# Kernel optimization log

Hardware: AMD Instinct MI355X
Metric: run time of the kernel (lower is better)

Reference implementation:

```python
import jax, jax.numpy as jnp
import numpy as np
from jax import lax

CHUNK = 4
HEADS = 8
SCALE = 16 ** -0.5  # key_dim ** -0.5


def _conv(x, w, pad=0, groups=1):
    return lax.conv_general_dilated(
        x, w, (1, 1), [(pad, pad), (pad, pad)],
        feature_group_count=groups,
        dimension_numbers=('NCHW', 'OIHW', 'NCHW'))


def _bn(x, g, b):
    # eval-mode BatchNorm with unit running stats folded to per-channel affine
    return x * g[:, None, None] + b[:, None, None]


def _shunt_row(x, c):  # torch shunted(..., dim=-1): [B,C,H,W] -> [B,c,C,H]
    B, C, H, W = x.shape
    return x.reshape(B, C, H, W // c, c).transpose(0, 4, 1, 2, 3).mean(-1)


def _shunt_col(x, c):  # torch shunted(..., dim=-2): [B,C,H,W] -> [B,c,C,W]
    B, C, H, W = x.shape
    return x.reshape(B, C, c, H // c, W).transpose(0, 2, 1, 3, 4).mean(-2)


def _posadd(x, pos):
    # F.interpolate(pos, size=N, mode='linear', align_corners=False)
    p = jax.image.resize(pos, (pos.shape[0], pos.shape[1], x.shape[-1]), 'linear')
    return x + p[None]


def _axial(sq, sk, sv, pq, pk):
    # sq/sk: [B,c,nh_kd,L], sv: [B,c,dh,L] -> out [B,c,h,L,d]
    B, c, _, L = sq.shape
    q = _posadd(sq, pq).reshape(B, c, HEADS, -1, L).transpose(0, 1, 2, 4, 3)  # [B,c,h,L,kd]
    k = _posadd(sk, pk).reshape(B, c, HEADS, -1, L)                            # [B,c,h,kd,L]
    v = sv.reshape(B, c, HEADS, -1, L).transpose(0, 1, 2, 4, 3)                # [B,c,h,L,d]
    attn = jax.nn.softmax(jnp.matmul(q, k) * SCALE, axis=-1)
    return jnp.matmul(attn, v)


def _forward(x, wcc, gcc, bcc, wen, gen, ben, sc, wq, gq, bq, wk, gk, bk,
             wv, gv, bv, wd, gd, bd, wp, gp, bp, wr, gr, br,
             wc2, gc2, bc2, wo, go, bo, prq, prk, pcq, pck):
    c = CHUNK
    # conv_ccam_b + ccam_enc
    cb = jax.nn.relu(_bn(_conv(x, wcc, pad=1), gcc, bcc))          # [B,128,H,W]
    cf = jax.nn.relu(_bn(_conv(cb, wen), gen, ben))                # [B,8,H,W]
    B, C, H, W = cb.shape
    # CCAMDec: bmm -> max-subtract -> softmax -> bmm -> scaled residual
    xf = cb.reshape(B, C, H * W)
    yf = cf.reshape(B, cf.shape[1], H * W)
    e = jnp.einsum('bcn,bkn->bck', xf, yf)
    a = jax.nn.softmax(e.max(-1, keepdims=True) - e, axis=-1)
    dec = jnp.einsum('bck,bkn->bcn', a, yf).reshape(B, C, H, W)
    xs = cb + sc[0] * dec
    # qkv projections
    q = _bn(_conv(xs, wq), gq, bq)   # [B,128,H,W]
    k = _bn(_conv(xs, wk), gk, bk)   # [B,128,H,W]
    v = _bn(_conv(xs, wv), gv, bv)   # [B,256,H,W]
    qkv = jnp.concatenate([q, k, v], axis=1)                       # [B,512,H,W]
    qkv = jax.nn.relu(_bn(_conv(qkv, wd, pad=1, groups=512), gd, bd))
    qkv = _bn(_conv(qkv, wp), gp, bp)                              # [B,128,H,W]
    DH = v.shape[1]
    # row axial attention
    xr = _axial(_shunt_row(q, c), _shunt_row(k, c), _shunt_row(v, c), prq, prk)  # [B,c,h,H,d]
    xr = xr.transpose(0, 2, 4, 1, 3).reshape(B, DH, c * c, H // c)
    xr = _bn(_conv(jax.nn.relu(xr), wr), gr, br)[..., None]        # [B,256,16,H/4,1]
    # column axial attention
    xc = _axial(_shunt_col(q, c), _shunt_col(k, c), _shunt_col(v, c), pcq, pck)  # [B,c,h,W,d]
    xc = xc.transpose(0, 2, 4, 1, 3).reshape(B, DH, c * c, W // c)
    xc = _bn(_conv(jax.nn.relu(xc), wc2), gc2, bc2)[:, :, :, None, :]  # [B,256,16,1,W/4]
    xx = (xr + xc).reshape(B, DH, H, W) + v
    # proj + h_sigmoid gate
    att = jnp.clip(_bn(_conv(jax.nn.relu(xx), wo), go, bo) + 3.0, 0.0, 6.0) / 6.0
    return att * qkv


def setup_inputs() -> dict:
    key = jax.random.key(0)
    ks = iter(jax.random.split(key, 40))
    nrm = lambda s, sd=0.05: jax.random.normal(next(ks), s, jnp.float32) * sd
    g = lambda n: 1.0 + 0.02 * jax.random.normal(next(ks), (n,), jnp.float32)
    b = lambda n: 0.02 * jax.random.normal(next(ks), (n,), jnp.float32)
    D, DH, NK = 128, 256, 128
    return dict(
        x=jax.random.normal(next(ks), (8, 64, 128, 128), jnp.float32),
        wcc=nrm((D, 64, 3, 3)), gcc=g(D), bcc=b(D),
        wen=nrm((8, D, 1, 1)), gen=g(8), ben=b(8),
        sc=jnp.array([0.5], jnp.float32),
        wq=nrm((NK, D, 1, 1)), gq=g(NK), bq=b(NK),
        wk=nrm((NK, D, 1, 1)), gk=g(NK), bk=b(NK),
        wv=nrm((DH, D, 1, 1)), gv=g(DH), bv=b(DH),
        wd=nrm((512, 1, 3, 3)), gd=g(512), bd=b(512),
        wp=nrm((D, 512, 1, 1)), gp=g(D), bp=b(D),
        wr=nrm((DH, DH, 1, 1)), gr=g(DH), br=b(DH),
        wc2=nrm((DH, DH, 1, 1)), gc2=g(DH), bc2=b(DH),
        wo=nrm((D, DH, 1, 1)), go=g(D), bo=b(D),
        prq=nrm((4, NK, 16), 1.0), prk=nrm((4, NK, 16), 1.0),
        pcq=nrm((4, NK, 16), 1.0), pck=nrm((4, NK, 16), 1.0),
    )


def reference(x, wcc, gcc, bcc, wen, gen, ben, sc, wq, gq, bq, wk, gk, bk,
              wv, gv, bv, wd, gd, bd, wp, gp, bp, wr, gr, br,
              wc2, gc2, bc2, wo, go, bo, prq, prk, pcq, pck):
    return _forward(x, wcc, gcc, bcc, wen, gen, ben, sc, wq, gq, bq, wk, gk, bk,
                    wv, gv, bv, wd, gd, bd, wp, gp, bp, wr, gr, br,
                    wc2, gc2, bc2, wo, go, bo, prq, prk, pcq, pck)
```

## Files before the change

kernel.cpp:

```cpp
#include <hip/hip_runtime.h>
#include <hip/hip_bf16.h>

typedef unsigned short u16;
typedef unsigned int u32;

#define DEVFN static __device__ __forceinline__

DEVFN float bfu(u32 u) { return __uint_as_float(u << 16); }
DEVFN u16 f2bu(float v) {
  u32 x = __float_as_uint(v);
  return (u16)((x + 0x7fffu + ((x >> 16) & 1u)) >> 16);
}

struct GemmP {
  const float* Xf;
  const float* W; const float* gain; const float* bias;
  float* outF; u16* outH; const float* aux;
  int CI; int N;
  const float* x3;
  const u16* dsrc; const float* wd; const float* gd; const float* bd;
  const float* xrc; const float* xcc;
};

template <int XM, int EP>
__launch_bounds__(256)
__global__ void gemm1x1(GemmP p) {
  __shared__ float Xs[16][64];
  __shared__ float Ws[16][64];
  const int b = blockIdx.z;
  const int n0 = blockIdx.x * 64;
  const int co0 = blockIdx.y * 64;
  const int t = threadIdx.x;
  const int tco = (t >> 4) << 2;
  const int tn = (t & 15) << 2;
  const int lk = t >> 4;
  const int ln = (t & 15) << 2;
  const int wc = t >> 2;
  const int wk = (t & 3) << 2;
  const int CI = p.CI, N = p.N;
  float acc[4][4] = {};

  for (int k0 = 0; k0 < CI; k0 += 16) {
    float v0, v1, v2, v3;
    if constexpr (XM == 0 || XM == 2) {
      const float* src = p.Xf + ((size_t)b * CI + (k0 + lk)) * N + n0 + ln;
      float4 r = *(const float4*)src;
      v0 = r.x; v1 = r.y; v2 = r.z; v3 = r.w;
      if constexpr (XM == 2) {
        v0 = fmaxf(v0, 0.f); v1 = fmaxf(v1, 0.f);
        v2 = fmaxf(v2, 0.f); v3 = fmaxf(v3, 0.f);
      }
    } else if constexpr (XM == 3) {
      const int k = k0 + lk;
      const int ci = k / 9;
      const int tap = k - ci * 9;
      const int dy = tap / 3 - 1;
      const int dx = tap - (tap / 3) * 3 - 1;
      const int y = (n0 >> 7) + dy;
      const int xb = (n0 & 127) + ln + dx;
      const float* src = p.x3 + ((size_t)b * 64 + ci) * 16384 + (size_t)y * 128;
      const bool yok = ((unsigned)y < 128u);
      v0 = (yok && (unsigned)(xb + 0) < 128u) ? src[xb + 0] : 0.f;
      v1 = (yok && (unsigned)(xb + 1) < 128u) ? src[xb + 1] : 0.f;
      v2 = (yok && (unsigned)(xb + 2) < 128u) ? src[xb + 2] : 0.f;
      v3 = (yok && (unsigned)(xb + 3) < 128u) ? src[xb + 3] : 0.f;
    } else if constexpr (XM == 4) {
      const int ci = k0 + lk;
      const int y = n0 >> 7;
      const int xb = (n0 & 127) + ln;
      const u16* src = p.dsrc + ((size_t)b * 512 + ci) * 16384;
      const float* wdp = p.wd + ci * 9;
      float s0 = 0.f, s1 = 0.f, s2 = 0.f, s3 = 0.f;
      #pragma unroll
      for (int dy = -1; dy <= 1; ++dy) {
        const int yy = y + dy;
        if ((unsigned)yy < 128u) {
          float tv[6];
          #pragma unroll
          for (int u = 0; u < 6; ++u) {
            const int xx = xb - 1 + u;
            tv[u] = ((unsigned)xx < 128u) ? bfu((u32)src[(size_t)yy * 128 + xx]) : 0.f;
          }
          const float w0 = wdp[(dy + 1) * 3 + 0];
          const float w1 = wdp[(dy + 1) * 3 + 1];
          const float w2 = wdp[(dy + 1) * 3 + 2];
          s0 += w0 * tv[0] + w1 * tv[1] + w2 * tv[2];
          s1 += w0 * tv[1] + w1 * tv[2] + w2 * tv[3];
          s2 += w0 * tv[2] + w1 * tv[3] + w2 * tv[4];
          s3 += w0 * tv[3] + w1 * tv[4] + w2 * tv[5];
        }
      }
      const float g = p.gd[ci], bb = p.bd[ci];
      v0 = fmaxf(g * s0 + bb, 0.f);
      v1 = fmaxf(g * s1 + bb, 0.f);
      v2 = fmaxf(g * s2 + bb, 0.f);
      v3 = fmaxf(g * s3 + bb, 0.f);
    } else {
      const int ch = k0 + lk;
      const int y = n0 >> 7;
      const int x0i = (n0 & 127) + ln;
      const int cc = y >> 3;
      const int abase = (y & 7) << 2;
      const u16* vsrc = p.dsrc + (((size_t)b * 512 + 256 + ch) * 128 + y) * 128;
      const float* xr = p.xrc + ((size_t)b * 256 + ch) * 512 + cc * 32;
      const float* xc = p.xcc + ((size_t)b * 256 + ch) * 512 + cc * 32;
      uint2 r = *(const uint2*)(vsrc + x0i);
      float vv0 = bfu(r.x & 0xffffu), vv1 = bfu(r.x >> 16);
      float vv2 = bfu(r.y & 0xffffu), vv3 = bfu(r.y >> 16);
      v0 = fmaxf(xr[abase + ((x0i + 0) >> 5)] + xc[(x0i + 0) & 31] + vv0, 0.f);
      v1 = fmaxf(xr[abase + ((x0i + 1) >> 5)] + xc[(x0i + 1) & 31] + vv1, 0.f);
      v2 = fmaxf(xr[abase + ((x0i + 2) >> 5)] + xc[(x0i + 2) & 31] + vv2, 0.f);
      v3 = fmaxf(xr[abase + ((x0i + 3) >> 5)] + xc[(x0i + 3) & 31] + vv3, 0.f);
    }
    Xs[lk][ln + 0] = v0; Xs[lk][ln + 1] = v1;
    Xs[lk][ln + 2] = v2; Xs[lk][ln + 3] = v3;
    {
      const float* src = p.W + (size_t)(co0 + wc) * CI + k0 + wk;
      float4 r = *(const float4*)src;
      Ws[wk + 0][wc] = r.x; Ws[wk + 1][wc] = r.y;
      Ws[wk + 2][wc] = r.z; Ws[wk + 3][wc] = r.w;
    }
    __syncthreads();
    #pragma unroll
    for (int kk = 0; kk < 16; ++kk) {
      const float4 a4 = *(const float4*)&Ws[kk][tco];
      const float4 b4 = *(const float4*)&Xs[kk][tn];
      acc[0][0] += a4.x * b4.x; acc[0][1] += a4.x * b4.y;
      acc[0][2] += a4.x * b4.z; acc[0][3] += a4.x * b4.w;
      acc[1][0] += a4.y * b4.x; acc[1][1] += a4.y * b4.y;
      acc[1][2] += a4.y * b4.z; acc[1][3] += a4.y * b4.w;
      acc[2][0] += a4.z * b4.x; acc[2][1] += a4.z * b4.y;
      acc[2][2] += a4.z * b4.z; acc[2][3] += a4.z * b4.w;
      acc[3][0] += a4.w * b4.x; acc[3][1] += a4.w * b4.y;
      acc[3][2] += a4.w * b4.z; acc[3][3] += a4.w * b4.w;
    }
    __syncthreads();
  }

  const int CO = (int)gridDim.y * 64;
  #pragma unroll
  for (int i = 0; i < 4; ++i) {
    const int co = co0 + tco + i;
    const float g = p.gain[co], bb = p.bias[co];
    const size_t oidx = ((size_t)b * CO + co) * N + n0 + tn;
    float o0 = g * acc[i][0] + bb;
    float o1 = g * acc[i][1] + bb;
    float o2 = g * acc[i][2] + bb;
    float o3 = g * acc[i][3] + bb;
    if constexpr (EP == 3) {
      o0 = fmaxf(o0, 0.f); o1 = fmaxf(o1, 0.f);
      o2 = fmaxf(o2, 0.f); o3 = fmaxf(o3, 0.f);
    }
    if constexpr (EP == 2) {
      const float4 ax = *(const float4*)(p.aux + oidx);
      o0 = fminf(fmaxf(o0 + 3.f, 0.f), 6.f) * (1.f / 6.f) * ax.x;
      o1 = fminf(fmaxf(o1 + 3.f, 0.f), 6.f) * (1.f / 6.f) * ax.y;
      o2 = fminf(fmaxf(o2 + 3.f, 0.f), 6.f) * (1.f / 6.f) * ax.z;
      o3 = fminf(fmaxf(o3 + 3.f, 0.f), 6.f) * (1.f / 6.f) * ax.w;
    }
    if constexpr (EP == 1) {
      u32 wlo = (u32)f2bu(o0) | ((u32)f2bu(o1) << 16);
      u32 whi = (u32)f2bu(o2) | ((u32)f2bu(o3) << 16);
      *(uint2*)(p.outH + oidx) = make_uint2(wlo, whi);
    } else {
      *(float4*)(p.outF + oidx) = make_float4(o0, o1, o2, o3);
    }
  }
}

__global__ void pack_qkv(const float* wq, const float* wk, const float* wv,
                         const float* gq, const float* bq,
                         const float* gk, const float* bk,
                         const float* gv, const float* bv,
                         float* W, float* g, float* b) {
  int t = blockIdx.x * 256 + threadIdx.x;
  if (t < 16384) { W[t] = wq[t]; W[16384 + t] = wk[t]; }
  W[32768 + t] = wv[t];
  if (t < 128) { g[t] = gq[t]; b[t] = bq[t]; g[128 + t] = gk[t]; b[128 + t] = bk[t]; }
  if (t < 256) { g[256 + t] = gv[t]; b[256 + t] = bv[t]; }
}

__global__ void cf_kernel(const float* cb, const float* wen, const float* gen,
                          const float* ben, float* cf) {
  __shared__ float w[8][128];
  const int t = threadIdx.x;
  for (int i = t; i < 1024; i += 256) w[i >> 7][i & 127] = wen[i];
  __syncthreads();
  const int b = blockIdx.y;
  const int n = blockIdx.x * 256 + t;
  const float* xb = cb + (size_t)b * 128 * 16384 + n;
  float acc[8] = {};
  for (int ci = 0; ci < 128; ++ci) {
    const float xv = xb[(size_t)ci * 16384];
    #pragma unroll
    for (int k = 0; k < 8; ++k) acc[k] += w[k][ci] * xv;
  }
  #pragma unroll
  for (int k = 0; k < 8; ++k)
    cf[((size_t)b * 8 + k) * 16384 + n] = fmaxf(gen[k] * acc[k] + ben[k], 0.f);
}

__global__ void ccam_attn(const float* cb, const float* cf, float* a) {
  const int b = blockIdx.x >> 7;
  const int c = blockIdx.x & 127;
  const int t = threadIdx.x;
  const float* xr = cb + ((size_t)b * 128 + c) * 16384;
  const float* yb = cf + (size_t)b * 8 * 16384;
  float pr[8] = {};
  for (int n = t; n < 16384; n += 256) {
    const float xv = xr[n];
    #pragma unroll
    for (int k = 0; k < 8; ++k) pr[k] += xv * yb[k * 16384 + n];
  }
  __shared__ float red[8][256];
  #pragma unroll
  for (int k = 0; k < 8; ++k) red[k][t] = pr[k];
  __syncthreads();
  for (int s = 128; s > 0; s >>= 1) {
    if (t < s) {
      #pragma unroll
      for (int k = 0; k < 8; ++k) red[k][t] += red[k][t + s];
    }
    __syncthreads();
  }
  if (t == 0) {
    float e[8], m = -1e30f;
    #pragma unroll
    for (int k = 0; k < 8; ++k) { e[k] = red[k][0]; m = fmaxf(m, e[k]); }
    float mt = -1e30f;
    #pragma unroll
    for (int k = 0; k < 8; ++k) mt = fmaxf(mt, m - e[k]);
    float s = 0.f, pk[8];
    #pragma unroll
    for (int k = 0; k < 8; ++k) { pk[k] = __expf(m - e[k] - mt); s += pk[k]; }
    const float inv = 1.f / s;
    #pragma unroll
    for (int k = 0; k < 8; ++k) a[((size_t)b * 128 + c) * 8 + k] = pk[k] * inv;
  }
}

__global__ void ccam_apply(float* cb, const float* cf, const float* a, const float* sc) {
  const int bc = blockIdx.y;
  const int b = bc >> 7;
  const int n = blockIdx.x * 256 + threadIdx.x;
  __shared__ float ak[8];
  if (threadIdx.x < 8) ak[threadIdx.x] = a[(size_t)bc * 8 + threadIdx.x];
  __syncthreads();
  const float* yb = cf + (size_t)b * 8 * 16384 + n;
  float dec = 0.f;
  #pragma unroll
  for (int k = 0; k < 8; ++k) dec += ak[k] * yb[k * 16384];
  const size_t idx = (size_t)bc * 16384 + n;
  cb[idx] = cb[idx] + sc[0] * dec;
}

__global__ void shunt_row(const u16* qkv, float* sr) {
  const int idx = blockIdx.x * 256 + threadIdx.x;
  const int h = idx & 127;
  const int c = (idx >> 7) & 511;
  const int b = idx >> 16;
  const uint4* src = (const uint4*)(qkv + (((size_t)b * 512 + c) * 128 + h) * 128);
  float s0 = 0.f, s1 = 0.f, s2 = 0.f, s3 = 0.f;
  #pragma unroll
  for (int w8 = 0; w8 < 16; ++w8) {
    const uint4 u = src[w8];
    s0 += bfu(u.x & 0xffffu) + bfu(u.z & 0xffffu);
    s1 += bfu(u.x >> 16)     + bfu(u.z >> 16);
    s2 += bfu(u.y & 0xffffu) + bfu(u.w & 0xffffu);
    s3 += bfu(u.y >> 16)     + bfu(u.w >> 16);
  }
  const size_t base = (((size_t)b * 4) * 512 + c) * 128 + h;
  sr[base + 0 * 512 * 128] = s0 * (1.f / 32.f);
  sr[base + 1 * 512 * 128] = s1 * (1.f / 32.f);
  sr[base + 2 * 512 * 128] = s2 * (1.f / 32.f);
  sr[base + 3 * 512 * 128] = s3 * (1.f / 32.f);
}

__global__ void shunt_col(const u16* qkv, float* scv) {
  const int idx = blockIdx.x * 256 + threadIdx.x;
  const int w = idx & 127;
  const int c = (idx >> 7) & 511;
  const int jc = (idx >> 16) & 3;
  const int b = idx >> 18;
  const u16* src = qkv + (((size_t)b * 512 + c) * 128 + jc * 32) * 128 + w;
  float s = 0.f;
  #pragma unroll
  for (int hr = 0; hr < 32; ++hr) s += bfu((u32)src[hr * 128]);
  scv[idx] = s * (1.f / 32.f);
}

DEVFN float pinterp(const float* pos, int j, int ch, int col) {
  const float s = (col + 0.5f) * 0.125f - 0.5f;
  const float fl = floorf(s);
  const int i0 = (int)fl;
  const float f = s - fl;
  const int ia = i0 < 0 ? 0 : (i0 > 15 ? 15 : i0);
  const int i1 = i0 + 1;
  const int ib = i1 < 0 ? 0 : (i1 > 15 ? 15 : i1);
  const float* pp = pos + ((size_t)j * 128 + ch) * 16;
  return pp[ia] * (1.f - f) + pp[ib] * f;
}

__global__ void axial(const float* sall, const float* posq, const float* posk,
                      float* out) {
  __shared__ float kl[16][128];
  __shared__ float vl[32][128];
  const int blk = blockIdx.x;
  const int h = blk & 7;
  const int jc = (blk >> 3) & 3;
  const int b = blk >> 5;
  const int r = threadIdx.x;
  const float* base = sall + ((size_t)b * 4 + jc) * 512 * 128;
  for (int i = r; i < 16 * 128; i += 128) {
    const int kd = i >> 7, col = i & 127;
    kl[kd][col] = base[(128 + h * 16 + kd) * 128 + col] + pinterp(posk, jc, h * 16 + kd, col);
  }
  for (int i = r; i < 32 * 128; i += 128) {
    const int d = i >> 7, col = i & 127;
    vl[d][col] = base[(256 + h * 32 + d) * 128 + col];
  }
  __syncthreads();
  float q[16];
  #pragma unroll
  for (int kd = 0; kd < 16; ++kd)
    q[kd] = base[(h * 16 + kd) * 128 + r] + pinterp(posq, jc, h * 16 + kd, r);
  float m = -1e30f;
  for (int col = 0; col < 128; ++col) {
    float s = 0.f;
    #pragma unroll
    for (int kd = 0; kd < 16; ++kd) s += q[kd] * kl[kd][col];
    m = fmaxf(m, s * 0.25f);
  }
  float den = 0.f;
  float acc[32] = {};
  for (int col = 0; col < 128; ++col) {
    float s = 0.f;
    #pragma unroll
    for (int kd = 0; kd < 16; ++kd) s += q[kd] * kl[kd][col];
    const float pv = __expf(s * 0.25f - m);
    den += pv;
    #pragma unroll
    for (int d = 0; d < 32; ++d) acc[d] += pv * vl[d][col];
  }
  const float inv = 1.f / den;
  float* ob = out + ((size_t)b * 256 + h * 32) * 512 + (size_t)jc * 128 + r;
  #pragma unroll
  for (int d = 0; d < 32; ++d) ob[(size_t)d * 512] = acc[d] * inv;
}

extern "C" void kernel_launch(void* const* d_in, const int* in_sizes, int n_in,
                              void* d_out, int out_size, void* d_ws, size_t ws_size,
                              hipStream_t stream) {
  const float* x   = (const float*)d_in[0];
  const float* wcc = (const float*)d_in[1];
  const float* gcc = (const float*)d_in[2];
  const float* bcc = (const float*)d_in[3];
  const float* wen = (const float*)d_in[4];
  const float* gen = (const float*)d_in[5];
  const float* ben = (const float*)d_in[6];
  const float* sc  = (const float*)d_in[7];
  const float* wq  = (const float*)d_in[8];
  const float* gq  = (const float*)d_in[9];
  const float* bq  = (const float*)d_in[10];
  const float* wk  = (const float*)d_in[11];
  const float* gk  = (const float*)d_in[12];
  const float* bk  = (const float*)d_in[13];
  const float* wv  = (const float*)d_in[14];
  const float* gv  = (const float*)d_in[15];
  const float* bv  = (const float*)d_in[16];
  const float* wd  = (const float*)d_in[17];
  const float* gd  = (const float*)d_in[18];
  const float* bd  = (const float*)d_in[19];
  const float* wp  = (const float*)d_in[20];
  const float* gp  = (const float*)d_in[21];
  const float* bp  = (const float*)d_in[22];
  const float* wr  = (const float*)d_in[23];
  const float* gr  = (const float*)d_in[24];
  const float* brr = (const float*)d_in[25];
  const float* wc2 = (const float*)d_in[26];
  const float* gc2 = (const float*)d_in[27];
  const float* bc2 = (const float*)d_in[28];
  const float* wo  = (const float*)d_in[29];
  const float* go  = (const float*)d_in[30];
  const float* bo  = (const float*)d_in[31];
  const float* prq = (const float*)d_in[32];
  const float* prk = (const float*)d_in[33];
  const float* pcq = (const float*)d_in[34];
  const float* pck = (const float*)d_in[35];

  char* ws = (char*)d_ws;
  u16*   qkv     = (u16*)  (ws + 0);
  char*  region  = ws + 134217728;
  float* cb      = (float*)region;
  float* sr_all  = (float*)(region + 0);
  float* sc_all  = (float*)(region + 8388608);
  float* xr_lin  = (float*)(region + 16777216);
  float* xc_lin  = (float*)(region + 20971520);
  float* xr_conv = (float*)(region + 25165824);
  float* xc_conv = (float*)(region + 29360128);
  float* cf      = (float*)(ws + 201326592);
  float* abuf    = (float*)(ws + 205520896);
  float* Wqkv    = (float*)(ws + 205553664);
  float* gqkv    = (float*)(ws + 205815808);
  float* bqkv    = (float*)(ws + 205817856);
  float* qkvp    = (float*)d_out;
  float* out     = (float*)d_out;

  pack_qkv<<<128, 256, 0, stream>>>(wq, wk, wv, gq, bq, gk, bk, gv, bv, Wqkv, gqkv, bqkv);

  { GemmP p{}; p.x3 = x; p.W = wcc; p.gain = gcc; p.bias = bcc; p.outF = cb;
    p.CI = 576; p.N = 16384;
    gemm1x1<3, 3><<<dim3(256, 2, 8), 256, 0, stream>>>(p); }

  cf_kernel<<<dim3(64, 8), 256, 0, stream>>>(cb, wen, gen, ben, cf);

  ccam_attn<<<1024, 256, 0, stream>>>(cb, cf, abuf);
  ccam_apply<<<dim3(64, 1024), 256, 0, stream>>>(cb, cf, abuf, sc);

  { GemmP p{}; p.Xf = cb; p.W = Wqkv; p.gain = gqkv; p.bias = bqkv; p.outH = qkv;
    p.CI = 128; p.N = 16384;
    gemm1x1<0, 1><<<dim3(256, 8, 8), 256, 0, stream>>>(p); }

  shunt_row<<<2048, 256, 0, stream>>>(qkv, sr_all);
  shunt_col<<<8192, 256, 0, stream>>>(qkv, sc_all);

  { GemmP p{}; p.dsrc = qkv; p.wd = wd; p.gd = gd; p.bd = bd;
    p.W = wp; p.gain = gp; p.bias = bp; p.outF = qkvp;
    p.CI = 512; p.N = 16384;
    gemm1x1<4, 0><<<dim3(256, 2, 8), 256, 0, stream>>>(p); }

  axial<<<256, 128, 0, stream>>>(sr_all, prq, prk, xr_lin);
  axial<<<256, 128, 0, stream>>>(sc_all, pcq, pck, xc_lin);

  { GemmP p{}; p.Xf = xr_lin; p.W = wr; p.gain = gr; p.bias = brr; p.outF = xr_conv;
    p.CI = 256; p.N = 512;
    gemm1x1<2, 0><<<dim3(8, 4, 8), 256, 0, stream>>>(p); }
  { GemmP p{}; p.Xf = xc_lin; p.W = wc2; p.gain = gc2; p.bias = bc2; p.outF = xc_conv;
    p.CI = 256; p.N = 512;
    gemm1x1<2, 0><<<dim3(8, 4, 8), 256, 0, stream>>>(p); }

  { GemmP p{}; p.dsrc = qkv; p.xrc = xr_conv; p.xcc = xc_conv;
    p.W = wo; p.gain = go; p.bias = bo; p.aux = qkvp; p.outF = out;
    p.CI = 256; p.N = 16384;
    gemm1x1<5, 2><<<dim3(256, 2, 8), 256, 0, stream>>>(p); }
}
```

Before: 1.724 ms.

## Rewrite pipeline with bf16 MFMA GEMMs and channel-last layout

Replaces the fp32 scalar-FMA 1x1/3x3 conv GEMMs with a bf16 MFMA (16x16x32) kernel and stores all intermediates in channel-last bf16. Weights are pre-packed to bf16, the input is transposed to NHWC, and the depthwise conv gets its own kernel, run per batch ahead of the projection GEMM. The CCAM reductions, shunt and axial kernels are also restructured. It cuts FP32 ALU work and memory traffic but adds bf16 rounding of intermediates and extra launches.

```diff
diff --git a/kernel.cpp b/kernel.cpp
--- a/kernel.cpp
+++ b/kernel.cpp
@@ -3,6 +3,8 @@
 
 typedef unsigned short u16;
 typedef unsigned int u32;
+typedef __attribute__((ext_vector_type(8))) short bf16x8;
+typedef __attribute__((ext_vector_type(4))) float f32x4;
 
 #define DEVFN static __device__ __forceinline__
 
@@ -11,282 +13,346 @@
   u32 x = __float_as_uint(v);
   return (u16)((x + 0x7fffu + ((x >> 16) & 1u)) >> 16);
 }
-
-struct GemmP {
-  const float* Xf;
-  const float* W; const float* gain; const float* bias;
-  float* outF; u16* outH; const float* aux;
-  int CI; int N;
-  const float* x3;
-  const u16* dsrc; const float* wd; const float* gd; const float* bd;
-  const float* xrc; const float* xcc;
+DEVFN float bfe(bf16x8 v, int j) { return bfu((u32)(u16)v[j]); }
+
+struct GP {
+  const u16* X; const u16* W;
+  const u16* Xv; const u16* Xr; const u16* Xc;
+  const u16* auxh;
+  u16* out; float* outf;
+  const float* gain; const float* bias;
+  int K; int NX; int CO; int b0;
 };
 
-template <int XM, int EP>
+template <int LD, int EP, int BM>
 __launch_bounds__(256)
-__global__ void gemm1x1(GemmP p) {
-  __shared__ float Xs[16][64];
-  __shared__ float Ws[16][64];
-  const int b = blockIdx.z;
-  const int n0 = blockIdx.x * 64;
-  const int co0 = blockIdx.y * 64;
+__global__ void gmm(GP p) {
+  __shared__ u16 Ws[64 * 72];
   const int t = threadIdx.x;
-  const int tco = (t >> 4) << 2;
-  const int tn = (t & 15) << 2;
-  const int lk = t >> 4;
-  const int ln = (t & 15) << 2;
-  const int wc = t >> 2;
-  const int wk = (t & 3) << 2;
-  const int CI = p.CI, N = p.N;
-  float acc[4][4] = {};
-
-  for (int k0 = 0; k0 < CI; k0 += 16) {
-    float v0, v1, v2, v3;
-    if constexpr (XM == 0 || XM == 2) {
-      const float* src = p.Xf + ((size_t)b * CI + (k0 + lk)) * N + n0 + ln;
-      float4 r = *(const float4*)src;
-      v0 = r.x; v1 = r.y; v2 = r.z; v3 = r.w;
-      if constexpr (XM == 2) {
-        v0 = fmaxf(v0, 0.f); v1 = fmaxf(v1, 0.f);
-        v2 = fmaxf(v2, 0.f); v3 = fmaxf(v3, 0.f);
-      }
-    } else if constexpr (XM == 3) {
-      const int k = k0 + lk;
-      const int ci = k / 9;
-      const int tap = k - ci * 9;
-      const int dy = tap / 3 - 1;
-      const int dx = tap - (tap / 3) * 3 - 1;
-      const int y = (n0 >> 7) + dy;
-      const int xb = (n0 & 127) + ln + dx;
-      const float* src = p.x3 + ((size_t)b * 64 + ci) * 16384 + (size_t)y * 128;
-      const bool yok = ((unsigned)y < 128u);
-      v0 = (yok && (unsigned)(xb + 0) < 128u) ? src[xb + 0] : 0.f;
-      v1 = (yok && (unsigned)(xb + 1) < 128u) ? src[xb + 1] : 0.f;
-      v2 = (yok && (unsigned)(xb + 2) < 128u) ? src[xb + 2] : 0.f;
-      v3 = (yok && (unsigned)(xb + 3) < 128u) ? src[xb + 3] : 0.f;
-    } else if constexpr (XM == 4) {
-      const int ci = k0 + lk;
-      const int y = n0 >> 7;
-      const int xb = (n0 & 127) + ln;
-      const u16* src = p.dsrc + ((size_t)b * 512 + ci) * 16384;
-      const float* wdp = p.wd + ci * 9;
-      float s0 = 0.f, s1 = 0.f, s2 = 0.f, s3 = 0.f;
-      #pragma unroll
-      for (int dy = -1; dy <= 1; ++dy) {
-        const int yy = y + dy;
+  const int lane = t & 63, wid = t >> 6;
+  const int wn = (wid >> 1) << 6;
+  const int wco = (wid & 1) << 5;
+  const int l15 = lane & 15, lg = lane >> 4;
+  const int n0 = blockIdx.x << 7;
+  const int co0 = blockIdx.y << 6;
+  const int b = (BM == 1) ? 0 : blockIdx.z;
+  const int bo = (BM == 1) ? p.b0 : blockIdx.z;
+  const int K = p.K;
+
+  f32x4 acc[4][2];
+  #pragma unroll
+  for (int f = 0; f < 4; ++f)
+    #pragma unroll
+    for (int c = 0; c < 2; ++c) acc[f][c] = (f32x4){0.f, 0.f, 0.f, 0.f};
+
+  const int sco = t >> 2, sks = (t & 3) << 4;
+  const u16* wrow = p.W + (size_t)(co0 + sco) * K + sks;
+
+  for (int kb = 0; kb < K; kb += 64) {
+    __syncthreads();
+    *(bf16x8*)&Ws[sco * 72 + sks] = *(const bf16x8*)(wrow + kb);
+    *(bf16x8*)&Ws[sco * 72 + sks + 8] = *(const bf16x8*)(wrow + kb + 8);
+    __syncthreads();
+    #pragma unroll
+    for (int ks = 0; ks < 64; ks += 32) {
+      const int k0 = kb + ks;
+      bf16x8 bfr[2];
+      bfr[0] = *(const bf16x8*)&Ws[(wco + l15) * 72 + ks + lg * 8];
+      bfr[1] = *(const bf16x8*)&Ws[(wco + 16 + l15) * 72 + ks + lg * 8];
+      bf16x8 af[4];
+      if constexpr (LD == 0) {
+        const size_t rb = (size_t)(b * p.NX + n0 + wn + l15);
+        #pragma unroll
+        for (int f = 0; f < 4; ++f)
+          af[f] = *(const bf16x8*)(p.X + (rb + f * 16) * K + k0 + lg * 8);
+      } else if constexpr (LD == 1) {
+        const int tap = k0 >> 6;
+        const int dy = tap / 3 - 1, dxt = tap - (tap / 3) * 3 - 1;
+        const int yy = blockIdx.x + dy;
+        const int ci0 = (k0 & 63) + lg * 8;
         if ((unsigned)yy < 128u) {
-          float tv[6];
           #pragma unroll
-          for (int u = 0; u < 6; ++u) {
-            const int xx = xb - 1 + u;
-            tv[u] = ((unsigned)xx < 128u) ? bfu((u32)src[(size_t)yy * 128 + xx]) : 0.f;
+          for (int f = 0; f < 4; ++f) {
+            const int xv = wn + f * 16 + l15 + dxt;
+            bf16x8 t8 = {};
+            if ((unsigned)xv < 128u)
+              t8 = *(const bf16x8*)(p.X + (((size_t)(b * 128 + yy) * 128 + xv) << 6) + ci0);
+            af[f] = t8;
           }
-          const float w0 = wdp[(dy + 1) * 3 + 0];
-          const float w1 = wdp[(dy + 1) * 3 + 1];
-          const float w2 = wdp[(dy + 1) * 3 + 2];
-          s0 += w0 * tv[0] + w1 * tv[1] + w2 * tv[2];
-          s1 += w0 * tv[1] + w1 * tv[2] + w2 * tv[3];
-          s2 += w0 * tv[2] + w1 * tv[3] + w2 * tv[4];
-          s3 += w0 * tv[3] + w1 * tv[4] + w2 * tv[5];
+        } else {
+          #pragma unroll
+          for (int f = 0; f < 4; ++f) af[f] = (bf16x8){};
+        }
+      } else {
+        const int y = blockIdx.x;
+        const int prb = ((y >> 3) << 5) + ((y & 7) << 2);
+        const int pcb = (y >> 3) << 5;
+        const int ch0 = k0 + lg * 8;
+        #pragma unroll
+        for (int f = 0; f < 4; ++f) {
+          const int x = wn + f * 16 + l15;
+          const int nn = n0 + x;
+          bf16x8 v8 = *(const bf16x8*)(p.Xv + ((size_t)(b * 16384 + nn) << 9) + 256 + ch0);
+          bf16x8 r8 = *(const bf16x8*)(p.Xr + ((size_t)(b * 512 + prb + (x >> 5)) << 8) + ch0);
+          bf16x8 c8 = *(const bf16x8*)(p.Xc + ((size_t)(b * 512 + pcb + (x & 31)) << 8) + ch0);
+          bf16x8 av;
+          #pragma unroll
+          for (int j = 0; j < 8; ++j) {
+            float s = bfe(v8, j) + bfe(r8, j) + bfe(c8, j);
+            av[j] = (short)f2bu(fmaxf(s, 0.f));
+          }
+          af[f] = av;
         }
       }
-      const float g = p.gd[ci], bb = p.bd[ci];
-      v0 = fmaxf(g * s0 + bb, 0.f);
-      v1 = fmaxf(g * s1 + bb, 0.f);
-      v2 = fmaxf(g * s2 + bb, 0.f);
-      v3 = fmaxf(g * s3 + bb, 0.f);
-    } else {
-      const int ch = k0 + lk;
-      const int y = n0 >> 7;
-      const int x0i = (n0 & 127) + ln;
-      const int cc = y >> 3;
-      const int abase = (y & 7) << 2;
-      const u16* vsrc = p.dsrc + (((size_t)b * 512 + 256 + ch) * 128 + y) * 128;
-      const float* xr = p.xrc + ((size_t)b * 256 + ch) * 512 + cc * 32;
-      const float* xc = p.xcc + ((size_t)b * 256 + ch) * 512 + cc * 32;
-      uint2 r = *(const uint2*)(vsrc + x0i);
-      float vv0 = bfu(r.x & 0xffffu), vv1 = bfu(r.x >> 16);
-      float vv2 = bfu(r.y & 0xffffu), vv3 = bfu(r.y >> 16);
-      v0 = fmaxf(xr[abase + ((x0i + 0) >> 5)] + xc[(x0i + 0) & 31] + vv0, 0.f);
-      v1 = fmaxf(xr[abase + ((x0i + 1) >> 5)] + xc[(x0i + 1) & 31] + vv1, 0.f);
-      v2 = fmaxf(xr[abase + ((x0i + 2) >> 5)] + xc[(x0i + 2) & 31] + vv2, 0.f);
-      v3 = fmaxf(xr[abase + ((x0i + 3) >> 5)] + xc[(x0i + 3) & 31] + vv3, 0.f);
-    }
-    Xs[lk][ln + 0] = v0; Xs[lk][ln + 1] = v1;
-    Xs[lk][ln + 2] = v2; Xs[lk][ln + 3] = v3;
-    {
-      const float* src = p.W + (size_t)(co0 + wc) * CI + k0 + wk;
-      float4 r = *(const float4*)src;
-      Ws[wk + 0][wc] = r.x; Ws[wk + 1][wc] = r.y;
-      Ws[wk + 2][wc] = r.z; Ws[wk + 3][wc] = r.w;
-    }
-    __syncthreads();
-    #pragma unroll
-    for (int kk = 0; kk < 16; ++kk) {
-      const float4 a4 = *(const float4*)&Ws[kk][tco];
-      const float4 b4 = *(const float4*)&Xs[kk][tn];
-      acc[0][0] += a4.x * b4.x; acc[0][1] += a4.x * b4.y;
-      acc[0][2] += a4.x * b4.z; acc[0][3] += a4.x * b4.w;
-      acc[1][0] += a4.y * b4.x; acc[1][1] += a4.y * b4.y;
-      acc[1][2] += a4.y * b4.z; acc[1][3] += a4.y * b4.w;
-      acc[2][0] += a4.z * b4.x; acc[2][1] += a4.z * b4.y;
-      acc[2][2] += a4.z * b4.z; acc[2][3] += a4.z * b4.w;
-      acc[3][0] += a4.w * b4.x; acc[3][1] += a4.w * b4.y;
-      acc[3][2] += a4.w * b4.z; acc[3][3] += a4.w * b4.w;
-    }
-    __syncthreads();
-  }
-
-  const int CO = (int)gridDim.y * 64;
-  #pragma unroll
-  for (int i = 0; i < 4; ++i) {
-    const int co = co0 + tco + i;
+      #pragma unroll
+      for (int f = 0; f < 4; ++f)
+        #pragma unroll
+        for (int c = 0; c < 2; ++c)
+          acc[f][c] = __builtin_amdgcn_mfma_f32_16x16x32_bf16(af[f], bfr[c], acc[f][c], 0, 0, 0);
+    }
+  }
+
+  #pragma unroll
+  for (int c = 0; c < 2; ++c) {
+    const int co = co0 + wco + (c << 4) + l15;
     const float g = p.gain[co], bb = p.bias[co];
-    const size_t oidx = ((size_t)b * CO + co) * N + n0 + tn;
-    float o0 = g * acc[i][0] + bb;
-    float o1 = g * acc[i][1] + bb;
-    float o2 = g * acc[i][2] + bb;
-    float o3 = g * acc[i][3] + bb;
-    if constexpr (EP == 3) {
-      o0 = fmaxf(o0, 0.f); o1 = fmaxf(o1, 0.f);
-      o2 = fmaxf(o2, 0.f); o3 = fmaxf(o3, 0.f);
-    }
-    if constexpr (EP == 2) {
-      const float4 ax = *(const float4*)(p.aux + oidx);
-      o0 = fminf(fmaxf(o0 + 3.f, 0.f), 6.f) * (1.f / 6.f) * ax.x;
-      o1 = fminf(fmaxf(o1 + 3.f, 0.f), 6.f) * (1.f / 6.f) * ax.y;
-      o2 = fminf(fmaxf(o2 + 3.f, 0.f), 6.f) * (1.f / 6.f) * ax.z;
-      o3 = fminf(fmaxf(o3 + 3.f, 0.f), 6.f) * (1.f / 6.f) * ax.w;
-    }
-    if constexpr (EP == 1) {
-      u32 wlo = (u32)f2bu(o0) | ((u32)f2bu(o1) << 16);
-      u32 whi = (u32)f2bu(o2) | ((u32)f2bu(o3) << 16);
-      *(uint2*)(p.outH + oidx) = make_uint2(wlo, whi);
-    } else {
-      *(float4*)(p.outF + oidx) = make_float4(o0, o1, o2, o3);
-    }
-  }
-}
-
-__global__ void pack_qkv(const float* wq, const float* wk, const float* wv,
-                         const float* gq, const float* bq,
-                         const float* gk, const float* bk,
-                         const float* gv, const float* bv,
-                         float* W, float* g, float* b) {
-  int t = blockIdx.x * 256 + threadIdx.x;
-  if (t < 16384) { W[t] = wq[t]; W[16384 + t] = wk[t]; }
-  W[32768 + t] = wv[t];
-  if (t < 128) { g[t] = gq[t]; b[t] = bq[t]; g[128 + t] = gk[t]; b[128 + t] = bk[t]; }
-  if (t < 256) { g[256 + t] = gv[t]; b[256 + t] = bv[t]; }
-}
-
-__global__ void cf_kernel(const float* cb, const float* wen, const float* gen,
-                          const float* ben, float* cf) {
-  __shared__ float w[8][128];
+    #pragma unroll
+    for (int f = 0; f < 4; ++f) {
+      const int nnb = n0 + wn + (f << 4) + (lg << 2);
+      #pragma unroll
+      for (int r = 0; r < 4; ++r) {
+        float o = g * acc[f][c][r] + bb;
+        const int nn = nnb + r;
+        if constexpr (EP == 1) o = fmaxf(o, 0.f);
+        if constexpr (EP == 2) {
+          o = fminf(fmaxf(o + 3.f, 0.f), 6.f) * (1.f / 6.f);
+          const float q = bfu((u32)p.auxh[((size_t)(bo * 16384 + nn) << 7) + co]);
+          p.outf[((size_t)(bo * 128 + co) << 14) + nn] = o * q;
+        } else {
+          p.out[(size_t)(bo * p.NX + nn) * p.CO + co] = f2bu(o);
+        }
+      }
+    }
+  }
+}
+
+__global__ void pack_k(const float* wcc, const float* wq, const float* wk, const float* wv,
+                       const float* gq, const float* gk, const float* gv,
+                       const float* bq, const float* bk, const float* bv,
+                       const float* wp, const float* wr, const float* wc2, const float* wo,
+                       u16* Wp3, u16* Wqkv, u16* Wwp, u16* Wwr, u16* Wwc, u16* Wwo,
+                       float* gqkv, float* bqkv, float* ebuf) {
+  int i = blockIdx.x * 256 + threadIdx.x;
+  if (i < 73728) {
+    const int co = i / 576, k = i - co * 576;
+    const int tap = k >> 6, ci = k & 63;
+    Wp3[i] = f2bu(wcc[(co * 64 + ci) * 9 + tap]);
+    return;
+  }
+  i -= 73728;
+  if (i < 65536) {
+    const int co = i >> 7, ci = i & 127;
+    const float v = co < 128 ? wq[co * 128 + ci]
+                  : (co < 256 ? wk[(co - 128) * 128 + ci] : wv[(co - 256) * 128 + ci]);
+    Wqkv[i] = f2bu(v);
+    return;
+  }
+  i -= 65536;
+  if (i < 65536) { Wwp[i] = f2bu(wp[i]); return; }
+  i -= 65536;
+  if (i < 65536) { Wwr[i] = f2bu(wr[i]); return; }
+  i -= 65536;
+  if (i < 65536) { Wwc[i] = f2bu(wc2[i]); return; }
+  i -= 65536;
+  if (i < 32768) { Wwo[i] = f2bu(wo[i]); return; }
+  i -= 32768;
+  if (i < 512) { gqkv[i] = i < 128 ? gq[i] : (i < 256 ? gk[i - 128] : gv[i - 256]); return; }
+  i -= 512;
+  if (i < 512) { bqkv[i] = i < 128 ? bq[i] : (i < 256 ? bk[i - 128] : bv[i - 256]); return; }
+  i -= 512;
+  if (i < 8192) ebuf[i] = 0.f;
+}
+
+__global__ void xt_k(const float* x, u16* xt) {
+  __shared__ u16 tile[64 * 130];
+  const int y = blockIdx.x, b = blockIdx.y;
   const int t = threadIdx.x;
-  for (int i = t; i < 1024; i += 256) w[i >> 7][i & 127] = wen[i];
+  {
+    const int ci = t >> 2, xseg = (t & 3) * 32;
+    const float* src = x + ((size_t)(b * 64 + ci) * 128 + y) * 128 + xseg;
+    #pragma unroll
+    for (int j = 0; j < 16; ++j) {
+      const float2 f2 = *(const float2*)(src + j * 2);
+      *(u32*)&tile[ci * 130 + xseg + 2 * j] = (u32)f2bu(f2.x) | ((u32)f2bu(f2.y) << 16);
+    }
+  }
   __syncthreads();
-  const int b = blockIdx.y;
+  const int xx = t >> 1, ch = (t & 1) * 32;
+  u16* dst = xt + (((size_t)(b * 128 + y) * 128 + xx) << 6) + ch;
+  uint4 q0, q1;
+  #pragma unroll
+  for (int h = 0; h < 2; ++h) {
+    const int cb0 = ch + h * 16;
+    u32 w0 = (u32)tile[(cb0 + 0) * 130 + xx] | ((u32)tile[(cb0 + 1) * 130 + xx] << 16);
+    u32 w1 = (u32)tile[(cb0 + 2) * 130 + xx] | ((u32)tile[(cb0 + 3) * 130 + xx] << 16);
+    u32 w2 = (u32)tile[(cb0 + 4) * 130 + xx] | ((u32)tile[(cb0 + 5) * 130 + xx] << 16);
+    u32 w3 = (u32)tile[(cb0 + 6) * 130 + xx] | ((u32)tile[(cb0 + 7) * 130 + xx] << 16);
+    u32 w4 = (u32)tile[(cb0 + 8) * 130 + xx] | ((u32)tile[(cb0 + 9) * 130 + xx] << 16);
+    u32 w5 = (u32)tile[(cb0 + 10) * 130 + xx] | ((u32)tile[(cb0 + 11) * 130 + xx] << 16);
+    u32 w6 = (u32)tile[(cb0 + 12) * 130 + xx] | ((u32)tile[(cb0 + 13) * 130 + xx] << 16);
+    u32 w7 = (u32)tile[(cb0 + 14) * 130 + xx] | ((u32)tile[(cb0 + 15) * 130 + xx] << 16);
+    if (h == 0) { q0 = make_uint4(w0, w1, w2, w3); q1 = make_uint4(w4, w5, w6, w7); }
+    else {
+      *(uint4*)(dst) = q0; *(uint4*)(dst + 8) = q1;
+      *(uint4*)(dst + 16) = make_uint4(w0, w1, w2, w3);
+      *(uint4*)(dst + 24) = make_uint4(w4, w5, w6, w7);
+    }
+  }
+}
+
+__global__ void cf_k(const u16* cb, const float* wen, const float* gen,
+                     const float* ben, u16* cf) {
+  __shared__ float wsm[1024];
+  const int t = threadIdx.x;
+  for (int i = t; i < 1024; i += 256) wsm[i] = wen[i];
+  __syncthreads();
   const int n = blockIdx.x * 256 + t;
-  const float* xb = cb + (size_t)b * 128 * 16384 + n;
+  const u16* row = cb + ((size_t)n << 7);
   float acc[8] = {};
-  for (int ci = 0; ci < 128; ++ci) {
-    const float xv = xb[(size_t)ci * 16384];
-    #pragma unroll
-    for (int k = 0; k < 8; ++k) acc[k] += w[k][ci] * xv;
-  }
-  #pragma unroll
-  for (int k = 0; k < 8; ++k)
-    cf[((size_t)b * 8 + k) * 16384 + n] = fmaxf(gen[k] * acc[k] + ben[k], 0.f);
-}
-
-__global__ void ccam_attn(const float* cb, const float* cf, float* a) {
-  const int b = blockIdx.x >> 7;
-  const int c = blockIdx.x & 127;
+  #pragma unroll 4
+  for (int i = 0; i < 16; ++i) {
+    const bf16x8 v = *(const bf16x8*)(row + i * 8);
+    #pragma unroll
+    for (int j = 0; j < 8; ++j) {
+      const float xv = bfe(v, j);
+      #pragma unroll
+      for (int k = 0; k < 8; ++k) acc[k] += wsm[k * 128 + i * 8 + j] * xv;
+    }
+  }
+  u32 o[4];
+  #pragma unroll
+  for (int k = 0; k < 4; ++k) {
+    const float a = fmaxf(gen[2 * k] * acc[2 * k] + ben[2 * k], 0.f);
+    const float bb = fmaxf(gen[2 * k + 1] * acc[2 * k + 1] + ben[2 * k + 1], 0.f);
+    o[k] = (u32)f2bu(a) | ((u32)f2bu(bb) << 16);
+  }
+  *(uint4*)(cf + ((size_t)n << 3)) = make_uint4(o[0], o[1], o[2], o[3]);
+}
+
+__global__ void ccam_e(const u16* cb, const u16* cf, float* ebuf) {
+  const int chunk = blockIdx.x, b = blockIdx.y;
   const int t = threadIdx.x;
-  const float* xr = cb + ((size_t)b * 128 + c) * 16384;
-  const float* yb = cf + (size_t)b * 8 * 16384;
-  float pr[8] = {};
-  for (int n = t; n < 16384; n += 256) {
-    const float xv = xr[n];
-    #pragma unroll
-    for (int k = 0; k < 8; ++k) pr[k] += xv * yb[k * 16384 + n];
-  }
-  __shared__ float red[8][256];
-  #pragma unroll
-  for (int k = 0; k < 8; ++k) red[k][t] = pr[k];
+  const int c = t & 127, kh = (t >> 7) * 4;
+  const int nb = b * 16384 + chunk * 512;
+  float a0 = 0.f, a1 = 0.f, a2 = 0.f, a3 = 0.f;
+  for (int i = 0; i < 512; ++i) {
+    const size_t n = (size_t)(nb + i);
+    const float xv = bfu((u32)cb[(n << 7) + c]);
+    const u32 p0 = *(const u32*)(cf + (n << 3) + kh);
+    const u32 p1 = *(const u32*)(cf + (n << 3) + kh + 2);
+    a0 += xv * bfu(p0 & 0xffffu);
+    a1 += xv * bfu(p0 >> 16);
+    a2 += xv * bfu(p1 & 0xffffu);
+    a3 += xv * bfu(p1 >> 16);
+  }
+  float* e = ebuf + ((size_t)(b * 128 + c) << 3) + kh;
+  atomicAdd(e + 0, a0); atomicAdd(e + 1, a1);
+  atomicAdd(e + 2, a2); atomicAdd(e + 3, a3);
+}
+
+__global__ void ccam_soft(const float* ebuf, float* abuf) {
+  const int b = blockIdx.x, c = threadIdx.x;
+  const float* e = ebuf + ((size_t)(b * 128 + c) << 3);
+  float ev[8], m = -1e30f;
+  #pragma unroll
+  for (int k = 0; k < 8; ++k) { ev[k] = e[k]; m = fmaxf(m, ev[k]); }
+  float mt = -1e30f;
+  #pragma unroll
+  for (int k = 0; k < 8; ++k) mt = fmaxf(mt, m - ev[k]);
+  float s = 0.f, pk[8];
+  #pragma unroll
+  for (int k = 0; k < 8; ++k) { pk[k] = __expf(m - ev[k] - mt); s += pk[k]; }
+  const float inv = 1.f / s;
+  float* a = abuf + ((size_t)(b * 128 + c) << 3);
+  #pragma unroll
+  for (int k = 0; k < 8; ++k) a[k] = pk[k] * inv;
+}
+
+__global__ void ccam_apply(const u16* cb, const u16* cf, const float* abuf,
+                           const float* sc, u16* xs) {
+  __shared__ float al[1024];
+  const int t = threadIdx.x;
+  const int gn0 = blockIdx.x * 128;
+  const int b = gn0 >> 14;
+  for (int i = t; i < 1024; i += 256) al[i] = abuf[(size_t)b * 1024 + i];
   __syncthreads();
-  for (int s = 128; s > 0; s >>= 1) {
-    if (t < s) {
+  const int n = gn0 + (t >> 1), ch = (t & 1) * 64;
+  const u16* crow = cb + ((size_t)n << 7) + ch;
+  u16* xrow = xs + ((size_t)n << 7) + ch;
+  const bf16x8 cf8 = *(const bf16x8*)(cf + ((size_t)n << 3));
+  float cfv[8];
+  #pragma unroll
+  for (int k = 0; k < 8; ++k) cfv[k] = bfe(cf8, k);
+  const float scv = sc[0];
+  #pragma unroll
+  for (int i = 0; i < 8; ++i) {
+    const bf16x8 cv = *(const bf16x8*)(crow + i * 8);
+    u32 o[4];
+    #pragma unroll
+    for (int jp = 0; jp < 4; ++jp) {
+      float r[2];
       #pragma unroll
-      for (int k = 0; k < 8; ++k) red[k][t] += red[k][t + s];
-    }
-    __syncthreads();
-  }
-  if (t == 0) {
-    float e[8], m = -1e30f;
-    #pragma unroll
-    for (int k = 0; k < 8; ++k) { e[k] = red[k][0]; m = fmaxf(m, e[k]); }
-    float mt = -1e30f;
-    #pragma unroll
-    for (int k = 0; k < 8; ++k) mt = fmaxf(mt, m - e[k]);
-    float s = 0.f, pk[8];
-    #pragma unroll
-    for (int k = 0; k < 8; ++k) { pk[k] = __expf(m - e[k] - mt); s += pk[k]; }
-    const float inv = 1.f / s;
-    #pragma unroll
-    for (int k = 0; k < 8; ++k) a[((size_t)b * 128 + c) * 8 + k] = pk[k] * inv;
-  }
-}
-
-__global__ void ccam_apply(float* cb, const float* cf, const float* a, const float* sc) {
-  const int bc = blockIdx.y;
-  const int b = bc >> 7;
-  const int n = blockIdx.x * 256 + threadIdx.x;
-  __shared__ float ak[8];
-  if (threadIdx.x < 8) ak[threadIdx.x] = a[(size_t)bc * 8 + threadIdx.x];
-  __syncthreads();
-  const float* yb = cf + (size_t)b * 8 * 16384 + n;
-  float dec = 0.f;
-  #pragma unroll
-  for (int k = 0; k < 8; ++k) dec += ak[k] * yb[k * 16384];
-  const size_t idx = (size_t)bc * 16384 + n;
-  cb[idx] = cb[idx] + sc[0] * dec;
+      for (int h = 0; h < 2; ++h) {
+        const int j = jp * 2 + h;
+        const float* ar = al + ((ch + i * 8 + j) << 3);
+        float dec = 0.f;
+        #pragma unroll
+        for (int k = 0; k < 8; ++k) dec += ar[k] * cfv[k];
+        r[h] = bfe(cv, j) + scv * dec;
+      }
+      o[jp] = (u32)f2bu(r[0]) | ((u32)f2bu(r[1]) << 16);
+    }
+    *(uint4*)(xrow + i * 8) = make_uint4(o[0], o[1], o[2], o[3]);
+  }
 }
 
 __global__ void shunt_row(const u16* qkv, float* sr) {
-  const int idx = blockIdx.x * 256 + threadIdx.x;
-  const int h = idx & 127;
-  const int c = (idx >> 7) & 511;
-  const int b = idx >> 16;
-  const uint4* src = (const uint4*)(qkv + (((size_t)b * 512 + c) * 128 + h) * 128);
-  float s0 = 0.f, s1 = 0.f, s2 = 0.f, s3 = 0.f;
-  #pragma unroll
-  for (int w8 = 0; w8 < 16; ++w8) {
-    const uint4 u = src[w8];
-    s0 += bfu(u.x & 0xffffu) + bfu(u.z & 0xffffu);
-    s1 += bfu(u.x >> 16)     + bfu(u.z >> 16);
-    s2 += bfu(u.y & 0xffffu) + bfu(u.w & 0xffffu);
-    s3 += bfu(u.y >> 16)     + bfu(u.w >> 16);
-  }
-  const size_t base = (((size_t)b * 4) * 512 + c) * 128 + h;
-  sr[base + 0 * 512 * 128] = s0 * (1.f / 32.f);
-  sr[base + 1 * 512 * 128] = s1 * (1.f / 32.f);
-  sr[base + 2 * 512 * 128] = s2 * (1.f / 32.f);
-  sr[base + 3 * 512 * 128] = s3 * (1.f / 32.f);
+  const int h = blockIdx.x, b = blockIdx.y;
+  const int c0 = threadIdx.x * 2;
+  float s0a = 0.f, s0b = 0.f, s1a = 0.f, s1b = 0.f;
+  float s2a = 0.f, s2b = 0.f, s3a = 0.f, s3b = 0.f;
+  for (int w4 = 0; w4 < 32; ++w4) {
+    const u16* rp = qkv + ((size_t)(b * 16384 + h * 128 + w4 * 4) << 9) + c0;
+    const u32 v0 = *(const u32*)(rp);
+    const u32 v1 = *(const u32*)(rp + 512);
+    const u32 v2 = *(const u32*)(rp + 1024);
+    const u32 v3 = *(const u32*)(rp + 1536);
+    s0a += bfu(v0 & 0xffffu); s0b += bfu(v0 >> 16);
+    s1a += bfu(v1 & 0xffffu); s1b += bfu(v1 >> 16);
+    s2a += bfu(v2 & 0xffffu); s2b += bfu(v2 >> 16);
+    s3a += bfu(v3 & 0xffffu); s3b += bfu(v3 >> 16);
+  }
+  const float iv = 1.f / 32.f;
+  *(float2*)(sr + ((size_t)((b * 4 + 0) * 128 + h) << 9) + c0) = make_float2(s0a * iv, s0b * iv);
+  *(float2*)(sr + ((size_t)((b * 4 + 1) * 128 + h) << 9) + c0) = make_float2(s1a * iv, s1b * iv);
+  *(float2*)(sr + ((size_t)((b * 4 + 2) * 128 + h) << 9) + c0) = make_float2(s2a * iv, s2b * iv);
+  *(float2*)(sr + ((size_t)((b * 4 + 3) * 128 + h) << 9) + c0) = make_float2(s3a * iv, s3b * iv);
 }
 
 __global__ void shunt_col(const u16* qkv, float* scv) {
-  const int idx = blockIdx.x * 256 + threadIdx.x;
-  const int w = idx & 127;
-  const int c = (idx >> 7) & 511;
-  const int jc = (idx >> 16) & 3;
-  const int b = idx >> 18;
-  const u16* src = qkv + (((size_t)b * 512 + c) * 128 + jc * 32) * 128 + w;
-  float s = 0.f;
-  #pragma unroll
-  for (int hr = 0; hr < 32; ++hr) s += bfu((u32)src[hr * 128]);
-  scv[idx] = s * (1.f / 32.f);
+  const int wseg = blockIdx.x, jc = blockIdx.y, b = blockIdx.z;
+  const int c0 = threadIdx.x * 2;
+  for (int wl = 0; wl < 16; ++wl) {
+    const int w = wseg * 16 + wl;
+    float sa = 0.f, sb = 0.f;
+    #pragma unroll 4
+    for (int hr = 0; hr < 32; ++hr) {
+      const u32 v = *(const u32*)(qkv + ((size_t)(b * 16384 + (jc * 32 + hr) * 128 + w) << 9) + c0);
+      sa += bfu(v & 0xffffu); sb += bfu(v >> 16);
+    }
+    *(float2*)(scv + ((size_t)((b * 4 + jc) * 128 + w) << 9) + c0) =
+        make_float2(sa * (1.f / 32.f), sb * (1.f / 32.f));
+  }
 }
 
 DEVFN float pinterp(const float* pos, int j, int ch, int col) {
@@ -301,29 +367,37 @@
   return pp[ia] * (1.f - f) + pp[ib] * f;
 }
 
-__global__ void axial(const float* sall, const float* posq, const float* posk,
-                      float* out) {
-  __shared__ float kl[16][128];
-  __shared__ float vl[32][128];
+__global__ void axial_k(const float* sall, const float* posq, const float* posk, u16* outp) {
+  __shared__ float kl[16][132];
+  __shared__ float vl[32][132];
   const int blk = blockIdx.x;
-  const int h = blk & 7;
-  const int jc = (blk >> 3) & 3;
-  const int b = blk >> 5;
+  const int h = blk & 7, jc = (blk >> 3) & 3, b = blk >> 5;
   const int r = threadIdx.x;
-  const float* base = sall + ((size_t)b * 4 + jc) * 512 * 128;
-  for (int i = r; i < 16 * 128; i += 128) {
-    const int kd = i >> 7, col = i & 127;
-    kl[kd][col] = base[(128 + h * 16 + kd) * 128 + col] + pinterp(posk, jc, h * 16 + kd, col);
-  }
-  for (int i = r; i < 32 * 128; i += 128) {
-    const int d = i >> 7, col = i & 127;
-    vl[d][col] = base[(256 + h * 32 + d) * 128 + col];
+  const float* myrow = sall + ((size_t)((b * 4 + jc) * 128 + r) << 9);
+  #pragma unroll
+  for (int i = 0; i < 4; ++i) {
+    const float4 kv = *(const float4*)(myrow + 128 + h * 16 + i * 4);
+    kl[i * 4 + 0][r] = kv.x + pinterp(posk, jc, h * 16 + i * 4 + 0, r);
+    kl[i * 4 + 1][r] = kv.y + pinterp(posk, jc, h * 16 + i * 4 + 1, r);
+    kl[i * 4 + 2][r] = kv.z + pinterp(posk, jc, h * 16 + i * 4 + 2, r);
+    kl[i * 4 + 3][r] = kv.w + pinterp(posk, jc, h * 16 + i * 4 + 3, r);
+  }
+  #pragma unroll
+  for (int i = 0; i < 8; ++i) {
+    const float4 vv = *(const float4*)(myrow + 256 + h * 32 + i * 4);
+    vl[i * 4 + 0][r] = vv.x; vl[i * 4 + 1][r] = vv.y;
+    vl[i * 4 + 2][r] = vv.z; vl[i * 4 + 3][r] = vv.w;
+  }
+  float q[16];
+  #pragma unroll
+  for (int i = 0; i < 4; ++i) {
+    const float4 qv = *(const float4*)(myrow + h * 16 + i * 4);
+    q[i * 4 + 0] = qv.x + pinterp(posq, jc, h * 16 + i * 4 + 0, r);
+    q[i * 4 + 1] = qv.y + pinterp(posq, jc, h * 16 + i * 4 + 1, r);
+    q[i * 4 + 2] = qv.z + pinterp(posq, jc, h * 16 + i * 4 + 2, r);
+    q[i * 4 + 3] = qv.w + pinterp(posq, jc, h * 16 + i * 4 + 3, r);
   }
   __syncthreads();
-  float q[16];
-  #pragma unroll
-  for (int kd = 0; kd < 16; ++kd)
-    q[kd] = base[(h * 16 + kd) * 128 + r] + pinterp(posq, jc, h * 16 + kd, r);
   float m = -1e30f;
   for (int col = 0; col < 128; ++col) {
     float s = 0.f;
@@ -343,9 +417,54 @@
     for (int d = 0; d < 32; ++d) acc[d] += pv * vl[d][col];
   }
   const float inv = 1.f / den;
-  float* ob = out + ((size_t)b * 256 + h * 32) * 512 + (size_t)jc * 128 + r;
-  #pragma unroll
-  for (int d = 0; d < 32; ++d) ob[(size_t)d * 512] = acc[d] * inv;
+  u16* ob = outp + (((size_t)(b * 512 + jc * 128 + r)) << 8) + h * 32;
+  #pragma unroll
+  for (int g8 = 0; g8 < 4; ++g8) {
+    u32 o[4];
+    #pragma unroll
+    for (int jp = 0; jp < 4; ++jp) {
+      const float a = fmaxf(acc[g8 * 8 + jp * 2 + 0] * inv, 0.f);
+      const float bb = fmaxf(acc[g8 * 8 + jp * 2 + 1] * inv, 0.f);
+      o[jp] = (u32)f2bu(a) | ((u32)f2bu(bb) << 16);
+    }
+    *(uint4*)(ob + g8 * 8) = make_uint4(o[0], o[1], o[2], o[3]);
+  }
+}
+
+__global__ void dw_k(const u16* qkv, const float* wd, const float* gd, const float* bd,
+                     u16* dwout, int b) {
+  const int xseg = blockIdx.x, y = blockIdx.y;
+  const int c0 = threadIdx.x * 2;
+  float w0[9], w1[9];
+  #pragma unroll
+  for (int tap = 0; tap < 9; ++tap) {
+    w0[tap] = wd[c0 * 9 + tap];
+    w1[tap] = wd[(c0 + 1) * 9 + tap];
+  }
+  const float g0 = gd[c0], g1 = gd[c0 + 1], b0 = bd[c0], b1 = bd[c0 + 1];
+  for (int xl = 0; xl < 32; ++xl) {
+    const int x = xseg * 32 + xl;
+    float s0 = 0.f, s1 = 0.f;
+    #pragma unroll
+    for (int dy = -1; dy <= 1; ++dy) {
+      const int yy = y + dy;
+      if ((unsigned)yy < 128u) {
+        #pragma unroll
+        for (int dxi = -1; dxi <= 1; ++dxi) {
+          const int xx = x + dxi;
+          if ((unsigned)xx < 128u) {
+            const u32 v = *(const u32*)(qkv + ((size_t)(b * 16384 + yy * 128 + xx) << 9) + c0);
+            const int tap = (dy + 1) * 3 + dxi + 1;
+            s0 += w0[tap] * bfu(v & 0xffffu);
+            s1 += w1[tap] * bfu(v >> 16);
+          }
+        }
+      }
+    }
+    const float o0 = fmaxf(g0 * s0 + b0, 0.f);
+    const float o1 = fmaxf(g1 * s1 + b1, 0.f);
+    *(u32*)(dwout + ((size_t)(y * 128 + x) << 9) + c0) = (u32)f2bu(o0) | ((u32)f2bu(o1) << 16);
+  }
 }
 
 extern "C" void kernel_launch(void* const* d_in, const int* in_sizes, int n_in,
@@ -389,58 +508,72 @@
   const float* pck = (const float*)d_in[35];
 
   char* ws = (char*)d_ws;
-  u16*   qkv     = (u16*)  (ws + 0);
-  char*  region  = ws + 134217728;
-  float* cb      = (float*)region;
-  float* sr_all  = (float*)(region + 0);
-  float* sc_all  = (float*)(region + 8388608);
-  float* xr_lin  = (float*)(region + 16777216);
-  float* xc_lin  = (float*)(region + 20971520);
-  float* xr_conv = (float*)(region + 25165824);
-  float* xc_conv = (float*)(region + 29360128);
-  float* cf      = (float*)(ws + 201326592);
-  float* abuf    = (float*)(ws + 205520896);
-  float* Wqkv    = (float*)(ws + 205553664);
-  float* gqkv    = (float*)(ws + 205815808);
-  float* bqkv    = (float*)(ws + 205817856);
-  float* qkvp    = (float*)d_out;
-  float* out     = (float*)d_out;
-
-  pack_qkv<<<128, 256, 0, stream>>>(wq, wk, wv, gq, bq, gk, bk, gv, bv, Wqkv, gqkv, bqkv);
-
-  { GemmP p{}; p.x3 = x; p.W = wcc; p.gain = gcc; p.bias = bcc; p.outF = cb;
-    p.CI = 576; p.N = 16384;
-    gemm1x1<3, 3><<<dim3(256, 2, 8), 256, 0, stream>>>(p); }
-
-  cf_kernel<<<dim3(64, 8), 256, 0, stream>>>(cb, wen, gen, ben, cf);
-
-  ccam_attn<<<1024, 256, 0, stream>>>(cb, cf, abuf);
-  ccam_apply<<<dim3(64, 1024), 256, 0, stream>>>(cb, cf, abuf, sc);
-
-  { GemmP p{}; p.Xf = cb; p.W = Wqkv; p.gain = gqkv; p.bias = bqkv; p.outH = qkv;
-    p.CI = 128; p.N = 16384;
-    gemm1x1<0, 1><<<dim3(256, 8, 8), 256, 0, stream>>>(p); }
-
-  shunt_row<<<2048, 256, 0, stream>>>(qkv, sr_all);
-  shunt_col<<<8192, 256, 0, stream>>>(qkv, sc_all);
-
-  { GemmP p{}; p.dsrc = qkv; p.wd = wd; p.gd = gd; p.bd = bd;
-    p.W = wp; p.gain = gp; p.bias = bp; p.outF = qkvp;
-    p.CI = 512; p.N = 16384;
-    gemm1x1<4, 0><<<dim3(256, 2, 8), 256, 0, stream>>>(p); }
-
-  axial<<<256, 128, 0, stream>>>(sr_all, prq, prk, xr_lin);
-  axial<<<256, 128, 0, stream>>>(sc_all, pcq, pck, xc_lin);
-
-  { GemmP p{}; p.Xf = xr_lin; p.W = wr; p.gain = gr; p.bias = brr; p.outF = xr_conv;
-    p.CI = 256; p.N = 512;
-    gemm1x1<2, 0><<<dim3(8, 4, 8), 256, 0, stream>>>(p); }
-  { GemmP p{}; p.Xf = xc_lin; p.W = wc2; p.gain = gc2; p.bias = bc2; p.outF = xc_conv;
-    p.CI = 256; p.N = 512;
-    gemm1x1<2, 0><<<dim3(8, 4, 8), 256, 0, stream>>>(p); }
-
-  { GemmP p{}; p.dsrc = qkv; p.xrc = xr_conv; p.xcc = xc_conv;
-    p.W = wo; p.gain = go; p.bias = bo; p.aux = qkvp; p.outF = out;
-    p.CI = 256; p.N = 16384;
-    gemm1x1<5, 2><<<dim3(256, 2, 8), 256, 0, stream>>>(p); }
-}
+  const size_t P = 134217728;
+  u16*   qkv    = (u16*)ws;
+  u16*   Wp3    = (u16*)(ws + 67108864);
+  u16*   cb     = (u16*)(ws + P);
+  float* sr_all = (float*)(ws + P);
+  float* sc_all = (float*)(ws + P + 8388608);
+  u16*   dwout  = (u16*)(ws + P);
+  u16*   xr_cv  = (u16*)(ws + P + 16777216);
+  u16*   xc_cv  = (u16*)(ws + P + 18874368);
+  u16*   xr_lin = (u16*)(ws + P + 20971520);
+  u16*   xc_lin = (u16*)(ws + P + 23068672);
+  u16*   xt     = (u16*)(ws + P + 33554432);
+  u16*   cfb    = (u16*)(ws + P + 33554432);
+  u16*   xs     = (u16*)(ws + P + 35651584);
+  u16*   qkvp   = (u16*)(ws + P + 35651584);
+  char*  WT     = ws + P + 69206016;
+  u16*   Wqkv   = (u16*)(WT);
+  u16*   Wwp    = (u16*)(WT + 131072);
+  u16*   Wwr    = (u16*)(WT + 262144);
+  u16*   Wwc    = (u16*)(WT + 393216);
+  u16*   Wwo    = (u16*)(WT + 524288);
+  float* gqkv   = (float*)(WT + 589824);
+  float* bqkv   = (float*)(WT + 591872);
+  float* ebuf   = (float*)(WT + 593920);
+  float* abuf   = (float*)(WT + 626688);
+  float* out    = (float*)d_out;
+
+  pack_k<<<1476, 256, 0, stream>>>(wcc, wq, wk, wv, gq, gk, gv, bq, bk, bv,
+                                   wp, wr, wc2, wo, Wp3, Wqkv, Wwp, Wwr, Wwc, Wwo,
+                                   gqkv, bqkv, ebuf);
+  xt_k<<<dim3(128, 8), 256, 0, stream>>>(x, xt);
+
+  { GP p{}; p.X = xt; p.W = Wp3; p.gain = gcc; p.bias = bcc; p.out = cb;
+    p.K = 576; p.NX = 16384; p.CO = 128;
+    gmm<1, 1, 0><<<dim3(128, 2, 8), 256, 0, stream>>>(p); }
+
+  cf_k<<<512, 256, 0, stream>>>(cb, wen, gen, ben, cfb);
+  ccam_e<<<dim3(32, 8), 256, 0, stream>>>(cb, cfb, ebuf);
+  ccam_soft<<<8, 128, 0, stream>>>(ebuf, abuf);
+  ccam_apply<<<1024, 256, 0, stream>>>(cb, cfb, abuf, sc, xs);
+
+  { GP p{}; p.X = xs; p.W = Wqkv; p.gain = gqkv; p.bias = bqkv; p.out = qkv;
+    p.K = 128; p.NX = 16384; p.CO = 512;
+    gmm<0, 0, 0><<<dim3(128, 8, 8), 256, 0, stream>>>(p); }
+
+  shunt_row<<<dim3(128, 8), 256, 0, stream>>>(qkv, sr_all);
+  shunt_col<<<dim3(8, 4, 8), 256, 0, stream>>>(qkv, sc_all);
+
+  axial_k<<<256, 128, 0, stream>>>(sr_all, prq, prk, xr_lin);
+  axial_k<<<256, 128, 0, stream>>>(sc_all, pcq, pck, xc_lin);
+  { GP p{}; p.X = xr_lin; p.W = Wwr; p.gain = gr; p.bias = brr; p.out = xr_cv;
+    p.K = 256; p.NX = 512; p.CO = 256;
+    gmm<0, 0, 0><<<dim3(4, 4, 8), 256, 0, stream>>>(p); }
+  { GP p{}; p.X = xc_lin; p.W = Wwc; p.gain = gc2; p.bias = bc2; p.out = xc_cv;
+    p.K = 256; p.NX = 512; p.CO = 256;
+    gmm<0, 0, 0><<<dim3(4, 4, 8), 256, 0, stream>>>(p); }
+
+  for (int bi = 0; bi < 8; ++bi) {
+    dw_k<<<dim3(4, 128), 256, 0, stream>>>(qkv, wd, gd, bd, dwout, bi);
+    GP p{}; p.X = dwout; p.W = Wwp; p.gain = gp; p.bias = bp; p.out = qkvp;
+    p.K = 512; p.NX = 16384; p.CO = 128; p.b0 = bi;
+    gmm<0, 0, 1><<<dim3(128, 2, 1), 256, 0, stream>>>(p);
+  }
+
+  { GP p{}; p.Xv = qkv; p.Xr = xr_cv; p.Xc = xc_cv; p.W = Wwo;
+    p.gain = go; p.bias = bo; p.auxh = qkvp; p.outf = out;
+    p.K = 256; p.NX = 16384; p.CO = 128;
+    gmm<2, 2, 0><<<dim3(128, 2, 8), 256, 0, stream>>>(p); }
+}
```

Measured after the change: 1.503 ms. 12.8% less time.
